# Kernel optimization log

Hardware: AMD Instinct MI355X
Metric: run time of the kernel (lower is better)

The kernel has to match this reference:

```python
import jax, jax.numpy as jnp
import numpy as np

B, H, W, C = 16, 56, 56, 384
NH, WS = 12, 7
N = WS * WS
NW = (H // WS) * (W // WS)
SHIFTS = (0, WS // 2)
HD = C // NH
SCALE = HD ** -0.5


def _rel_idx():
    ch, cw = np.meshgrid(np.arange(WS), np.arange(WS), indexing='ij')
    cf = np.stack([ch.ravel(), cw.ravel()])            # (2, N)
    rc = cf[:, :, None] - cf[:, None, :]               # (2, N, N)
    rc = rc.transpose(1, 2, 0).copy()
    rc[:, :, 0] += WS - 1
    rc[:, :, 1] += WS - 1
    rc[:, :, 0] *= 2 * WS - 1
    return rc.sum(-1).astype(np.int32)                 # (N, N)


def _attn_mask(shift):
    img = np.zeros((H, W))
    sl = (slice(0, -WS), slice(-WS, -shift), slice(-shift, None))
    cnt = 0
    for hs in sl:
        for ws_ in sl:
            img[hs, ws_] = cnt
            cnt += 1
    mw = img.reshape(H // WS, WS, W // WS, WS).transpose(0, 2, 1, 3).reshape(-1, N)
    d = mw[:, None, :] - mw[:, :, None]
    return np.where(d != 0, -100.0, 0.0).astype(np.float32)  # (NW, N, N)


def setup_inputs() -> dict:
    key = jax.random.key(0)
    ks = jax.random.split(key, 8)
    p = lambda k, shape: (jax.random.normal(k, shape, jnp.float32) * 0.02)
    return dict(
        x=jax.random.normal(ks[0], (B, H, W, C), jnp.float32),
        attn_mask=jnp.asarray(_attn_mask(SHIFTS[1])),
        rel_idx=jnp.asarray(_rel_idx()),
        norm1_g=jnp.ones((2, C), jnp.float32),
        norm1_b=jnp.zeros((2, C), jnp.float32),
        qkv_w=p(ks[1], (2, 3 * C, C)),
        qkv_b=jnp.zeros((2, 3 * C), jnp.float32),
        rpb=p(ks[2], (2, (2 * WS - 1) ** 2, NH)),
        proj_w=p(ks[3], (2, C, C)),
        proj_b=jnp.zeros((2, C), jnp.float32),
        norm2_g=jnp.ones((2, C), jnp.float32),
        norm2_b=jnp.zeros((2, C), jnp.float32),
        fc1_w=p(ks[4], (2, 4 * C, C)),
        fc1_b=jnp.zeros((2, 4 * C), jnp.float32),
        fc2_w=p(ks[5], (2, C, 4 * C)),
        fc2_b=jnp.zeros((2, C), jnp.float32),
    )


def _ln(x, g, b):
    m = x.mean(-1, keepdims=True)
    v = x.var(-1, keepdims=True)
    return (x - m) * jax.lax.rsqrt(v + 1e-5) * g + b


def _partition(x):
    # (B,H,W,C) -> (B*nW, N, C)
    x = x.reshape(B, H // WS, WS, W // WS, WS, C)
    return x.transpose(0, 1, 3, 2, 4, 5).reshape(-1, N, C)


def _reverse(w):
    # (B*nW, N, C) -> (B,H,W,C)
    w = w.reshape(B, H // WS, W // WS, WS, WS, C)
    return w.transpose(0, 1, 3, 2, 4, 5).reshape(B, H, W, C)


def reference(x, attn_mask, rel_idx, norm1_g, norm1_b, qkv_w, qkv_b, rpb,
              proj_w, proj_b, norm2_g, norm2_b, fc1_w, fc1_b, fc2_w, fc2_b):
    for i, shift in enumerate(SHIFTS):
        shortcut = x.reshape(B, H * W, C)
        xn = _ln(shortcut, norm1_g[i], norm1_b[i]).reshape(B, H, W, C)
        if shift > 0:
            xn = jnp.roll(xn, (-shift, -shift), (1, 2))
        xw = _partition(xn)                               # (B_, N, C)
        qkv = xw @ qkv_w[i].T + qkv_b[i]                  # (B_, N, 3C)
        qkv = qkv.reshape(-1, N, 3, NH, HD).transpose(2, 0, 3, 1, 4)
        q, k, v = qkv[0], qkv[1], qkv[2]                  # (B_, NH, N, HD)
        attn = jnp.einsum('bhnd,bhmd->bhnm', q * SCALE, k)
        bias = rpb[i][rel_idx.reshape(-1)].reshape(N, N, NH).transpose(2, 0, 1)
        attn = attn + bias[None]
        if shift > 0:
            attn = attn.reshape(B, NW, NH, N, N) + attn_mask[None, :, None]
            attn = attn.reshape(-1, NH, N, N)
        attn = jax.nn.softmax(attn, axis=-1)
        out = jnp.einsum('bhnm,bhmd->bhnd', attn, v)
        out = out.transpose(0, 2, 1, 3).reshape(-1, N, C)
        out = out @ proj_w[i].T + proj_b[i]
        sx = _reverse(out)
        if shift > 0:
            sx = jnp.roll(sx, (shift, shift), (1, 2))
        x = shortcut + sx.reshape(B, H * W, C)
        h = jax.nn.gelu(_ln(x, norm2_g[i], norm2_b[i]) @ fc1_w[i].T + fc1_b[i],
                        approximate=False)
        x = x + (h @ fc2_w[i].T + fc2_b[i])
        x = x.reshape(B, H, W, C)
    return x
```

## Files before the change

kernel.cpp:

```cpp
#include <hip/hip_runtime.h>
#include <math.h>

typedef unsigned short u16;
typedef unsigned int   u32;
typedef __attribute__((ext_vector_type(4))) float f32x4;
typedef __attribute__((ext_vector_type(8))) short bf16x8;

#define M_TOK 50176
#define CDIM  384

__device__ __forceinline__ u16 f2b(float f){
  union { float f; u32 u; } v; v.f = f;
  u32 r = v.u + 0x7fffu + ((v.u >> 16) & 1u);
  return (u16)(r >> 16);
}
__device__ __forceinline__ u32 pack2(float a, float b){
  return (u32)f2b(a) | ((u32)f2b(b) << 16);
}

__device__ __forceinline__ void gload_lds16(const u16* g, u16* l){
  __builtin_amdgcn_global_load_lds((const __attribute__((address_space(1))) u32*)g,
                                   (__attribute__((address_space(3))) u32*)l, 16, 0, 0);
}

__global__ void cvtw(const float* __restrict__ in, u16* __restrict__ out, int n4){
  int i = blockIdx.x * 256 + threadIdx.x;
  if (i < n4){
    float4 v = ((const float4*)in)[i];
    uint2 o; o.x = pack2(v.x, v.y); o.y = pack2(v.z, v.w);
    ((uint2*)out)[i] = o;
  }
}

__global__ __launch_bounds__(256) void ln_kernel(
    const float* __restrict__ x, const float* __restrict__ g,
    const float* __restrict__ b, u16* __restrict__ out, int ntok)
{
  int wave = threadIdx.x >> 6, lane = threadIdx.x & 63;
  for (long t = blockIdx.x * 4 + wave; t < ntok; t += (long)gridDim.x * 4){
    const float* xr = x + t * CDIM;
    float v[6]; float s = 0.f, ss = 0.f;
    #pragma unroll
    for (int j = 0; j < 6; ++j){ v[j] = xr[j*64 + lane]; s += v[j]; ss += v[j]*v[j]; }
    #pragma unroll
    for (int o = 32; o >= 1; o >>= 1){ s += __shfl_xor(s, o); ss += __shfl_xor(ss, o); }
    float mean = s * (1.f/384.f);
    float var  = ss * (1.f/384.f) - mean*mean;
    float rs   = rsqrtf(var + 1e-5f);
    #pragma unroll
    for (int j = 0; j < 6; ++j){
      int c = j*64 + lane;
      out[t*CDIM + c] = f2b((v[j] - mean) * rs * g[c] + b[c]);
    }
  }
}

template<int EPI>
__global__ __launch_bounds__(256, 4) void gemm_bt(
    const u16* __restrict__ A, const u16* __restrict__ Wt,
    const float* __restrict__ bias, const float* __restrict__ resid,
    void* __restrict__ outp, int M, int N, int K)
{
  __shared__ __align__(16) u16 lA[2][128*32];
  __shared__ __align__(16) u16 lB[2][128*32];
  const int tid  = threadIdx.x;
  const int wave = tid >> 6, lane = tid & 63;
  const int bn = blockIdx.x, bm = blockIdx.y;
  const int wr = wave >> 1, wc = wave & 1;
  const int l15 = lane & 15, l4 = lane >> 4;
  const int srow = tid >> 2, sch = tid & 3;

  f32x4 acc[4][4] = {};

  auto STAGE = [&](int buf, int kt){
    #pragma unroll
    for (int it = 0; it < 2; ++it){
      int row = it*64 + srow;
      int chs = sch ^ ((srow >> 1) & 3);
      const u16* ga = A  + (size_t)(bm*128 + row) * K + kt + chs*8;
      const u16* gb = Wt + (size_t)(bn*128 + row) * K + kt + chs*8;
      gload_lds16(ga, &lA[buf][(it*256 + wave*64) * 8]);
      gload_lds16(gb, &lB[buf][(it*256 + wave*64) * 8]);
    }
  };

  const int NK = K >> 5;
  STAGE(0, 0);

  int cur = 0;
  for (int ki = 0; ki < NK; ++ki){
    if (ki + 1 < NK){
      STAGE(cur ^ 1, (ki + 1) * 32);
      asm volatile("s_waitcnt vmcnt(4)" ::: "memory");
    } else {
      asm volatile("s_waitcnt vmcnt(0)" ::: "memory");
    }
    __builtin_amdgcn_s_barrier();
    bf16x8 af[4], bfr[4];
    const int rc = (l4 ^ ((l15 >> 1) & 3)) * 8;
    #pragma unroll
    for (int mi = 0; mi < 4; ++mi)
      af[mi] = *(const bf16x8*)&lA[cur][(wr*64 + mi*16 + l15)*32 + rc];
    #pragma unroll
    for (int ni = 0; ni < 4; ++ni)
      bfr[ni] = *(const bf16x8*)&lB[cur][(wc*64 + ni*16 + l15)*32 + rc];
    #pragma unroll
    for (int mi = 0; mi < 4; ++mi)
      #pragma unroll
      for (int ni = 0; ni < 4; ++ni)
        acc[mi][ni] = __builtin_amdgcn_mfma_f32_16x16x32_bf16(af[mi], bfr[ni], acc[mi][ni], 0, 0, 0);
    __builtin_amdgcn_s_barrier();
    cur ^= 1;
  }

  #pragma unroll
  for (int ni = 0; ni < 4; ++ni){
    int col = bn*128 + wc*64 + ni*16 + l15;
    float bb = bias[col];
    #pragma unroll
    for (int mi = 0; mi < 4; ++mi){
      int row0 = bm*128 + wr*64 + mi*16 + l4*4;
      #pragma unroll
      for (int r = 0; r < 4; ++r){
        long off = (long)(row0 + r) * N + col;
        float v = acc[mi][ni][r] + bb;
        if (EPI == 0){
          ((u16*)outp)[off] = f2b(v);
        } else if (EPI == 1){
          ((u16*)outp)[off] = f2b(0.5f * v * (1.f + erff(v * 0.70710678118654752f)));
        } else {
          ((float*)outp)[off] = resid[off] + v;
        }
      }
    }
  }
}

__global__ void build_btbl(const float* __restrict__ rpb, const int* __restrict__ ridx,
                           float* __restrict__ btbl){
  int q = blockIdx.x & 63, h = blockIdx.x >> 6;
  int l = threadIdx.x;
  float v = -1e9f;
  if (q < 49){
    int key = (l & 3) * 16 + (l >> 2);
    if (key < 49) v = rpb[ridx[q*49 + key] * 12 + h];
  }
  btbl[(h*64 + q)*64 + l] = v;
}

template<int SHIFT>
__global__ __launch_bounds__(64) void attn_mfma(
    const u16* __restrict__ qkv,
    const float* __restrict__ btbl,
    u16* __restrict__ attn_out)
{
  __shared__ __align__(16) u16 p_lds[64*72];
  __shared__ __align__(16) u16 vt_lds[32*72];
  __shared__ int tok_lds[64];
  __shared__ int rid_lds[64];

  const int bid = blockIdx.x;
  const int h   = bid % 12;
  const int win = bid / 12;
  const int b   = win >> 6, wl = win & 63;
  const int wy  = wl >> 3,  wx = wl & 7;
  const int lane = threadIdx.x;
  const int l15 = lane & 15, l4 = lane >> 4;

  auto tokof = [&](int n)->int{
    int r = (n * 9363) >> 16;
    int c = n - r * 7;
    int hh = wy*7 + r + SHIFT; if (hh >= 56) hh -= 56;
    int ww = wx*7 + c + SHIFT; if (ww >= 56) ww -= 56;
    return b*3136 + hh*56 + ww;
  };

  {
    const int n  = lane;
    const int nc = n < 49 ? n : 48;
    const int t  = tokof(nc);
    tok_lds[n] = t;
    if (SHIFT){
      int r = (nc * 9363) >> 16, c = nc - r*7;
      int gh = wy*7 + r, gw = wx*7 + c;
      int rh = gh <= 48 ? 0 : (gh <= 52 ? 1 : 2);
      int rw = gw <= 48 ? 0 : (gw <= 52 ? 1 : 2);
      rid_lds[n] = rh*3 + rw;
    }
    const uint4* vp = (const uint4*)(qkv + (size_t)t*1152 + 768 + h*32);
    u32 w[16];
    #pragma unroll
    for (int j4 = 0; j4 < 4; ++j4){
      uint4 u = vp[j4];
      w[j4*4+0]=u.x; w[j4*4+1]=u.y; w[j4*4+2]=u.z; w[j4*4+3]=u.w;
    }
    if (n >= 49){
      #pragma unroll
      for (int j = 0; j < 16; ++j) w[j] = 0;
    }
    #pragma unroll
    for (int j = 0; j < 16; ++j){
      vt_lds[(2*j  )*72 + n] = (u16)(w[j] & 0xffffu);
      vt_lds[(2*j+1)*72 + n] = (u16)(w[j] >> 16);
    }
  }

  bf16x8 qa[4], kb[4];
  #pragma unroll
  for (int mi = 0; mi < 4; ++mi){
    int row = mi*16 + l15; int t = tokof(row < 49 ? row : 48);
    qa[mi] = *(const bf16x8*)(qkv + (size_t)t*1152 + h*32 + l4*8);
  }
  #pragma unroll
  for (int ni = 0; ni < 4; ++ni){
    int row = ni*16 + l15; int t = tokof(row < 49 ? row : 48);
    kb[ni] = *(const bf16x8*)(qkv + (size_t)t*1152 + 384 + h*32 + l4*8);
  }
  f32x4 s[4][4] = {};
  #pragma unroll
  for (int mi = 0; mi < 4; ++mi)
    #pragma unroll
    for (int ni = 0; ni < 4; ++ni)
      s[mi][ni] = __builtin_amdgcn_mfma_f32_16x16x32_bf16(qa[mi], kb[ni], s[mi][ni], 0, 0, 0);

  __syncthreads();

  int rid_k[4];
  if (SHIFT){
    #pragma unroll
    for (int ni = 0; ni < 4; ++ni) rid_k[ni] = rid_lds[ni*16 + l15];
  }

  const float* bt = btbl + h*4096;
  float den[4][4];
  #pragma unroll
  for (int mi = 0; mi < 4; ++mi){
    #pragma unroll
    for (int r = 0; r < 4; ++r){
      int q = mi*16 + l4*4 + r;
      f32x4 bq = *(const f32x4*)(bt + q*64 + l15*4);
      int ridq = 0;
      if (SHIFT) ridq = rid_lds[q];
      #pragma unroll
      for (int ni = 0; ni < 4; ++ni){
        float v = s[mi][ni][r] * 0.17677669529663687f + bq[ni];
        if (SHIFT) v += (ridq == rid_k[ni]) ? 0.f : -100.f;
        s[mi][ni][r] = v;
      }
      float m0 = fmaxf(fmaxf(s[mi][0][r], s[mi][1][r]), fmaxf(s[mi][2][r], s[mi][3][r]));
      #pragma unroll
      for (int o = 1; o <= 8; o <<= 1) m0 = fmaxf(m0, __shfl_xor(m0, o));
      float d0 = 0.f;
      #pragma unroll
      for (int ni = 0; ni < 4; ++ni){
        float e = __expf(s[mi][ni][r] - m0);
        s[mi][ni][r] = e; d0 += e;
      }
      #pragma unroll
      for (int o = 1; o <= 8; o <<= 1) d0 += __shfl_xor(d0, o);
      den[mi][r] = d0;
    }
  }

  #pragma unroll
  for (int mi = 0; mi < 4; ++mi)
    #pragma unroll
    for (int r = 0; r < 4; ++r){
      int q = mi*16 + l4*4 + r;
      #pragma unroll
      for (int ni = 0; ni < 4; ++ni)
        p_lds[q*72 + ni*16 + l15] = f2b(s[mi][ni][r]);
    }

  __syncthreads();

  f32x4 o2[4][2] = {};
  #pragma unroll
  for (int ks = 0; ks < 2; ++ks){
    bf16x8 vb[2];
    #pragma unroll
    for (int ni = 0; ni < 2; ++ni)
      vb[ni] = *(const bf16x8*)&vt_lds[(ni*16 + l15)*72 + ks*32 + l4*8];
    #pragma unroll
    for (int mi = 0; mi < 4; ++mi){
      bf16x8 pa = *(const bf16x8*)&p_lds[(mi*16 + l15)*72 + ks*32 + l4*8];
      #pragma unroll
      for (int ni = 0; ni < 2; ++ni)
        o2[mi][ni] = __builtin_amdgcn_mfma_f32_16x16x32_bf16(pa, vb[ni], o2[mi][ni], 0, 0, 0);
    }
  }

  #pragma unroll
  for (int mi = 0; mi < 4; ++mi){
    #pragma unroll
    for (int r = 0; r < 4; ++r){
      int q = mi*16 + l4*4 + r;
      if (q < 49){
        float inv = 1.f / den[mi][r];
        long t = tok_lds[q];
        #pragma unroll
        for (int ni = 0; ni < 2; ++ni){
          int d = ni*16 + l15;
          attn_out[t*384 + h*32 + d] = f2b(o2[mi][ni][r] * inv);
        }
      }
    }
  }
}

extern "C" void kernel_launch(void* const* d_in, const int* in_sizes, int n_in,
                              void* d_out, int out_size, void* d_ws, size_t ws_size,
                              hipStream_t stream)
{
  const float* x_in   = (const float*)d_in[0];
  const int*   relidx = (const int*)d_in[2];
  const float* n1g    = (const float*)d_in[3];
  const float* n1b    = (const float*)d_in[4];
  const float* qkvw   = (const float*)d_in[5];
  const float* qkvb   = (const float*)d_in[6];
  const float* rpb    = (const float*)d_in[7];
  const float* pw     = (const float*)d_in[8];
  const float* pb     = (const float*)d_in[9];
  const float* n2g    = (const float*)d_in[10];
  const float* n2b    = (const float*)d_in[11];
  const float* f1w    = (const float*)d_in[12];
  const float* f1b    = (const float*)d_in[13];
  const float* f2w    = (const float*)d_in[14];
  const float* f2bb   = (const float*)d_in[15];
  float* xout = (float*)d_out;

  char* ws = (char*)d_ws;
  u16* wqkv  = (u16*)ws; ws += (size_t)2*1152*384*2;
  u16* wproj = (u16*)ws; ws += (size_t)2*384*384*2;
  u16* wfc1  = (u16*)ws; ws += (size_t)2*1536*384*2;
  u16* wfc2  = (u16*)ws; ws += (size_t)2*384*1536*2;
  u16* bufA  = (u16*)ws; ws += (size_t)M_TOK*1536*2;
  u16* bufB  = (u16*)ws; ws += (size_t)M_TOK*384*2;
  float* btbl = (float*)(bufA + (size_t)M_TOK*1152);

  {
    int n;
    n = 2*1152*384;  cvtw<<<dim3((n/4+255)/256), dim3(256), 0, stream>>>(qkvw, wqkv, n/4);
    n = 2*384*384;   cvtw<<<dim3((n/4+255)/256), dim3(256), 0, stream>>>(pw,   wproj, n/4);
    n = 2*1536*384;  cvtw<<<dim3((n/4+255)/256), dim3(256), 0, stream>>>(f1w,  wfc1, n/4);
    n = 2*384*1536;  cvtw<<<dim3((n/4+255)/256), dim3(256), 0, stream>>>(f2w,  wfc2, n/4);
  }

  for (int i = 0; i < 2; ++i){
    const float* xi = (i == 0) ? x_in : xout;
    ln_kernel<<<dim3(2048), dim3(256), 0, stream>>>(xi, n1g + i*384, n1b + i*384, bufB, M_TOK);
    gemm_bt<0><<<dim3(9, 392), dim3(256), 0, stream>>>(
        bufB, wqkv + (size_t)i*1152*384, qkvb + i*1152, nullptr, bufA, M_TOK, 1152, 384);
    build_btbl<<<dim3(768), dim3(64), 0, stream>>>(rpb + (size_t)i*169*12, relidx, btbl);
    if (i == 0)
      attn_mfma<0><<<dim3(12288), dim3(64), 0, stream>>>(bufA, btbl, bufB);
    else
      attn_mfma<3><<<dim3(12288), dim3(64), 0, stream>>>(bufA, btbl, bufB);
    gemm_bt<2><<<dim3(3, 392), dim3(256), 0, stream>>>(
        bufB, wproj + (size_t)i*384*384, pb + i*384, xi, xout, M_TOK, 384, 384);
    ln_kernel<<<dim3(2048), dim3(256), 0, stream>>>(xout, n2g + i*384, n2b + i*384, bufB, M_TOK);
    gemm_bt<1><<<dim3(12, 392), dim3(256), 0, stream>>>(
        bufB, wfc1 + (size_t)i*1536*384, f1b + i*1536, nullptr, bufA, M_TOK, 1536, 384);
    gemm_bt<2><<<dim3(3, 392), dim3(256), 0, stream>>>(
        bufA, wfc2 + (size_t)i*384*1536, f2bb + i*384, xout, xout, M_TOK, 384, 1536);
  }
  (void)in_sizes; (void)n_in; (void)out_size; (void)ws_size;
}
```

Measured before the change: 1.052 ms.

## Remap GEMM blocks across XCDs and stage bf16 epilogue through LDS

The GEMM launch becomes a 1D grid, and block ids are remapped so each group of 8 (one per XCD in round-robin dispatch) gets a contiguous chunk of tiles, which is meant to improve L2 reuse of shared A/W rows. For the bf16-output epilogues (QKV and FC1+GELU), results are first written to a swizzled LDS tile and then stored as coalesced 32-bit words per row, replacing scattered 2-byte global stores. The fp32 residual epilogue is unchanged. The extra __syncthreads and LDS round trip add some cost, and the remap assumes the grid size is divisible by 8.

```diff
diff --git a/kernel.cpp b/kernel.cpp
--- a/kernel.cpp
+++ b/kernel.cpp
@@ -61,11 +61,13 @@
     const float* __restrict__ bias, const float* __restrict__ resid,
     void* __restrict__ outp, int M, int N, int K)
 {
-  __shared__ __align__(16) u16 lA[2][128*32];
-  __shared__ __align__(16) u16 lB[2][128*32];
+  __shared__ __align__(16) u16 smem[16384];
   const int tid  = threadIdx.x;
   const int wave = tid >> 6, lane = tid & 63;
-  const int bn = blockIdx.x, bm = blockIdx.y;
+  const int nbn  = N >> 7;
+  const int cpx  = gridDim.x >> 3;
+  const int sid  = (blockIdx.x & 7) * cpx + (blockIdx.x >> 3);
+  const int bm = sid / nbn, bn = sid % nbn;
   const int wr = wave >> 1, wc = wave & 1;
   const int l15 = lane & 15, l4 = lane >> 4;
   const int srow = tid >> 2, sch = tid & 3;
@@ -73,14 +75,16 @@
   f32x4 acc[4][4] = {};
 
   auto STAGE = [&](int buf, int kt){
+    u16* lAp = smem + buf*4096;
+    u16* lBp = smem + 8192 + buf*4096;
     #pragma unroll
     for (int it = 0; it < 2; ++it){
       int row = it*64 + srow;
       int chs = sch ^ ((srow >> 1) & 3);
       const u16* ga = A  + (size_t)(bm*128 + row) * K + kt + chs*8;
       const u16* gb = Wt + (size_t)(bn*128 + row) * K + kt + chs*8;
-      gload_lds16(ga, &lA[buf][(it*256 + wave*64) * 8]);
-      gload_lds16(gb, &lB[buf][(it*256 + wave*64) * 8]);
+      gload_lds16(ga, &lAp[(it*256 + wave*64) * 8]);
+      gload_lds16(gb, &lBp[(it*256 + wave*64) * 8]);
     }
   };
 
@@ -96,14 +100,16 @@
       asm volatile("s_waitcnt vmcnt(0)" ::: "memory");
     }
     __builtin_amdgcn_s_barrier();
+    const u16* lAp = smem + cur*4096;
+    const u16* lBp = smem + 8192 + cur*4096;
     bf16x8 af[4], bfr[4];
     const int rc = (l4 ^ ((l15 >> 1) & 3)) * 8;
     #pragma unroll
     for (int mi = 0; mi < 4; ++mi)
-      af[mi] = *(const bf16x8*)&lA[cur][(wr*64 + mi*16 + l15)*32 + rc];
+      af[mi] = *(const bf16x8*)&lAp[(wr*64 + mi*16 + l15)*32 + rc];
     #pragma unroll
     for (int ni = 0; ni < 4; ++ni)
-      bfr[ni] = *(const bf16x8*)&lB[cur][(wc*64 + ni*16 + l15)*32 + rc];
+      bfr[ni] = *(const bf16x8*)&lBp[(wc*64 + ni*16 + l15)*32 + rc];
     #pragma unroll
     for (int mi = 0; mi < 4; ++mi)
       #pragma unroll
@@ -113,25 +119,47 @@
     cur ^= 1;
   }
 
-  #pragma unroll
-  for (int ni = 0; ni < 4; ++ni){
-    int col = bn*128 + wc*64 + ni*16 + l15;
-    float bb = bias[col];
-    #pragma unroll
-    for (int mi = 0; mi < 4; ++mi){
-      int row0 = bm*128 + wr*64 + mi*16 + l4*4;
-      #pragma unroll
-      for (int r = 0; r < 4; ++r){
-        long off = (long)(row0 + r) * N + col;
-        float v = acc[mi][ni][r] + bb;
-        if (EPI == 0){
-          ((u16*)outp)[off] = f2b(v);
-        } else if (EPI == 1){
-          ((u16*)outp)[off] = f2b(0.5f * v * (1.f + erff(v * 0.70710678118654752f)));
-        } else {
-          ((float*)outp)[off] = resid[off] + v;
+  if (EPI == 2){
+    #pragma unroll
+    for (int ni = 0; ni < 4; ++ni){
+      int col = bn*128 + wc*64 + ni*16 + l15;
+      float bb = bias[col];
+      #pragma unroll
+      for (int mi = 0; mi < 4; ++mi){
+        int row0 = bm*128 + wr*64 + mi*16 + l4*4;
+        #pragma unroll
+        for (int r = 0; r < 4; ++r){
+          long off = (long)(row0 + r) * N + col;
+          ((float*)outp)[off] = resid[off] + acc[mi][ni][r] + bb;
         }
       }
+    }
+  } else {
+    #pragma unroll
+    for (int ni = 0; ni < 4; ++ni){
+      int colL = wc*64 + ni*16 + l15;
+      float bb = bias[bn*128 + colL];
+      int colS = colL ^ (l4*16);
+      #pragma unroll
+      for (int mi = 0; mi < 4; ++mi){
+        int rowL = wr*64 + mi*16 + l4*4;
+        #pragma unroll
+        for (int r = 0; r < 4; ++r){
+          float v = acc[mi][ni][r] + bb;
+          if (EPI == 1) v = 0.5f * v * (1.f + erff(v * 0.70710678118654752f));
+          smem[(rowL + r)*128 + colS] = f2b(v);
+        }
+      }
+    }
+    __syncthreads();
+    const u32* eb = (const u32*)smem;
+    u32* og = (u32*)outp;
+    const int nW = N >> 1;
+    #pragma unroll
+    for (int it = 0; it < 32; ++it){
+      int row = wave*32 + it;
+      u32 w = eb[row*64 + (lane ^ (((row >> 2) & 3) * 8))];
+      og[(size_t)(bm*128 + row) * nW + bn*64 + lane] = w;
     }
   }
 }
@@ -349,19 +377,19 @@
   for (int i = 0; i < 2; ++i){
     const float* xi = (i == 0) ? x_in : xout;
     ln_kernel<<<dim3(2048), dim3(256), 0, stream>>>(xi, n1g + i*384, n1b + i*384, bufB, M_TOK);
-    gemm_bt<0><<<dim3(9, 392), dim3(256), 0, stream>>>(
+    gemm_bt<0><<<dim3(3528), dim3(256), 0, stream>>>(
         bufB, wqkv + (size_t)i*1152*384, qkvb + i*1152, nullptr, bufA, M_TOK, 1152, 384);
     build_btbl<<<dim3(768), dim3(64), 0, stream>>>(rpb + (size_t)i*169*12, relidx, btbl);
     if (i == 0)
       attn_mfma<0><<<dim3(12288), dim3(64), 0, stream>>>(bufA, btbl, bufB);
     else
       attn_mfma<3><<<dim3(12288), dim3(64), 0, stream>>>(bufA, btbl, bufB);
-    gemm_bt<2><<<dim3(3, 392), dim3(256), 0, stream>>>(
+    gemm_bt<2><<<dim3(1176), dim3(256), 0, stream>>>(
         bufB, wproj + (size_t)i*384*384, pb + i*384, xi, xout, M_TOK, 384, 384);
     ln_kernel<<<dim3(2048), dim3(256), 0, stream>>>(xout, n2g + i*384, n2b + i*384, bufB, M_TOK);
-    gemm_bt<1><<<dim3(12, 392), dim3(256), 0, stream>>>(
+    gemm_bt<1><<<dim3(4704), dim3(256), 0, stream>>>(
         bufB, wfc1 + (size_t)i*1536*384, f1b + i*1536, nullptr, bufA, M_TOK, 1536, 384);
-    gemm_bt<2><<<dim3(3, 392), dim3(256), 0, stream>>>(
+    gemm_bt<2><<<dim3(1176), dim3(256), 0, stream>>>(
         bufA, wfc2 + (size_t)i*384*1536, f2bb + i*384, xout, xout, M_TOK, 384, 1536);
   }
   (void)in_sizes; (void)n_in; (void)out_size; (void)ws_size;
```

After: 967.7 us. -8.0%, faster.
